# Optimization experiments

Hardware: AMD Instinct MI355X
Metric: run time of the kernel (lower is better)

## Reference

```python
import jax, jax.numpy as jnp
import numpy as np

B, L, D_MODEL, H = 2, 2048, 1024, 16
D_HEAD = D_MODEL // H
NEG = -1e9


def setup_inputs() -> dict:
    key = jax.random.key(0)
    ks = jax.random.split(key, 8)
    q = jax.random.normal(ks[0], (B, L, D_MODEL), dtype=jnp.float32)
    k = jax.random.normal(ks[1], (B, L, D_MODEL), dtype=jnp.float32)
    v = jax.random.normal(ks[2], (B, L, D_MODEL), dtype=jnp.float32)
    # causal mask: True where attention is disallowed (masked_fill semantics)
    mask = jnp.broadcast_to(jnp.triu(jnp.ones((L, L), dtype=bool), k=1), (B, L, L))
    s = 1.0 / np.sqrt(D_MODEL)
    Wq = jax.random.normal(ks[3], (D_MODEL, D_MODEL), dtype=jnp.float32) * s
    Wk = jax.random.normal(ks[4], (D_MODEL, D_MODEL), dtype=jnp.float32) * s
    Wv = jax.random.normal(ks[5], (D_MODEL, D_MODEL), dtype=jnp.float32) * s
    Wo = jax.random.normal(ks[6], (D_MODEL, D_MODEL), dtype=jnp.float32) * s
    return {"q": q, "k": k, "v": v, "mask": mask,
            "Wq": Wq, "Wk": Wk, "Wv": Wv, "Wo": Wo}


def reference(q, k, v, mask, Wq, Wk, Wv, Wo):
    # projections (Linear, bias=False)
    qh = (q @ Wq).reshape(B, L, H, D_HEAD)
    kh = (k @ Wk).reshape(B, L, H, D_HEAD)
    vh = (v @ Wv).reshape(B, L, H, D_HEAD)
    # per-head scores: contiguous d_model slices == head reshape
    scores = jnp.einsum("bqhd,bkhd->bhqk", qh, kh)
    scores = jnp.where(mask[:, None, :, :], NEG, scores)
    # NOTE: original applies softmax FIRST, then divides by sqrt(d_head)
    weights = jax.nn.softmax(scores, axis=-1) / np.sqrt(D_HEAD).astype(np.float32)
    att = jnp.einsum("bhqk,bkhd->bqhd", weights, vh).reshape(B, L, D_MODEL)
    # dropout is identity in eval mode
    return att @ Wo
```

## Files before the change

### kernel.cpp

```cpp
#include <hip/hip_runtime.h>
#include <hip/hip_bf16.h>

#define BATCH  2
#define SEQ    2048
#define DMODEL 1024
#define NHEAD  16
#define DHEAD  64

typedef _Float16 f16x4 __attribute__((ext_vector_type(4)));
typedef _Float16 f16x8 __attribute__((ext_vector_type(8)));
typedef float    f32x4 __attribute__((ext_vector_type(4)));

union H16 { unsigned short u; _Float16 f; };
__device__ __forceinline__ _Float16 u2h(unsigned short u) { H16 c; c.u = u; return c.f; }
__device__ __forceinline__ unsigned short h2u(_Float16 f) { H16 c; c.f = f; return c.u; }

__device__ __forceinline__ void gll16(const void* g, void* l) {
    __builtin_amdgcn_global_load_lds(
        (const __attribute__((address_space(1))) void*)g,
        (__attribute__((address_space(3))) void*)l, 16, 0, 0);
}

__device__ __forceinline__ float dpp_max16(float x) {
    float t;
    t = __int_as_float(__builtin_amdgcn_update_dpp(0, __float_as_int(x), 0xB1, 0xF, 0xF, true));
    x = fmaxf(x, t);
    t = __int_as_float(__builtin_amdgcn_update_dpp(0, __float_as_int(x), 0x4E, 0xF, 0xF, true));
    x = fmaxf(x, t);
    t = __int_as_float(__builtin_amdgcn_update_dpp(0, __float_as_int(x), 0x124, 0xF, 0xF, true));
    x = fmaxf(x, t);
    t = __int_as_float(__builtin_amdgcn_update_dpp(0, __float_as_int(x), 0x128, 0xF, 0xF, true));
    x = fmaxf(x, t);
    return x;
}

__device__ __forceinline__ void pack_body(const float* __restrict__ W,
                                          _Float16* __restrict__ Phi,
                                          _Float16* __restrict__ Plo)
{
    const int n0 = blockIdx.x * 64;
    const int k0 = blockIdx.y * 64;
    const int t  = threadIdx.x;
    const int nl = t & 63;
    const int kc = (t >> 6) * 16;
    const int n  = n0 + nl;
    const int sw = (n & 3) ^ ((n >> 2) & 3);

    _Float16 hi[16], lo[16];
#pragma unroll
    for (int i = 0; i < 16; i++) {
        float x = W[(size_t)(k0 + kc + i) * DMODEL + n] * 32.0f;
        _Float16 h = (_Float16)x;
        hi[i] = h;
        lo[i] = (_Float16)(x - (float)h);
    }
#pragma unroll
    for (int cc = 0; cc < 2; cc++) {
        const int kk = kc + cc * 8;
        const int g  = kk >> 5;
        const int c  = (kk >> 3) & 3;
        const size_t off = (size_t)n * DMODEL + k0 + g * 32 + ((c ^ sw) << 3);
        *(f16x8*)&Phi[off] = *(f16x8*)&hi[cc * 8];
        if (Plo) *(f16x8*)&Plo[off] = *(f16x8*)&lo[cc * 8];
    }
}

__global__ __launch_bounds__(256) void pack_qkv(const float* __restrict__ Wq,
                                                const float* __restrict__ Wk,
                                                const float* __restrict__ Wv,
                                                _Float16* qhiT, _Float16* qloT,
                                                _Float16* khiT, _Float16* kloT,
                                                _Float16* vhiT)
{
    const int z = blockIdx.z;
    pack_body(z == 0 ? Wq : z == 1 ? Wk : Wv,
              z == 0 ? qhiT : z == 1 ? khiT : vhiT,
              z == 0 ? qloT : z == 1 ? kloT : nullptr);
}

__global__ __launch_bounds__(256) void pack_one(const float* __restrict__ W,
                                                _Float16* Phi)
{
    pack_body(W, Phi, nullptr);
}

template <int SPLIT, typename CT>
__global__ __launch_bounds__(256) void gemm_mfma(const float* __restrict__ A0,
                                                 const float* __restrict__ A1,
                                                 const _Float16* __restrict__ Bh0,
                                                 const _Float16* __restrict__ Bl0,
                                                 const _Float16* __restrict__ Bh1,
                                                 const _Float16* __restrict__ Bl1,
                                                 CT* __restrict__ C0,
                                                 CT* __restrict__ C1,
                                                 _Float16* __restrict__ Kh,
                                                 _Float16* __restrict__ Kl,
                                                 int N, int K)
{
    constexpr int ASZ = 128 * 40;
    constexpr int BSZ = 128 * 32;
    constexpr int AHI = 0;
    constexpr int ALO = ASZ;
    constexpr int BHI = ASZ * (SPLIT == 3 ? 2 : 1);
    constexpr int BLO = BHI + 2 * BSZ;
    constexpr int TOT = BHI + 2 * BSZ * (SPLIT == 3 ? 2 : 1);
    __shared__ __align__(16) _Float16 smem[TOT];

    const float*    A  = blockIdx.z ? A1 : A0;
    const _Float16* Bh = blockIdx.z ? Bh1 : Bh0;
    const _Float16* Bl = blockIdx.z ? Bl1 : Bl0;
    CT*             C  = blockIdx.z ? C1 : C0;

    const int m0 = blockIdx.x * 128;
    const int n0 = blockIdx.y * 128;
    const int t    = threadIdx.x;
    const int wave = t >> 6;
    const int lane = t & 63;
    const int quad = lane >> 4;
    const int col  = lane & 15;
    const int wm   = (wave & 1) * 64;
    const int wn   = (wave >> 1) * 64;

    const int ar  = t >> 1;
    const int akc = (t & 1) * 16;
    const float* Ap = A + (size_t)(m0 + ar) * K + akc;

    const _Float16* BhSrc = Bh + (size_t)(n0 + wave * 32 + (lane >> 2)) * K + (lane & 3) * 8;
    const _Float16* BlSrc = (SPLIT == 3)
        ? Bl + (size_t)(n0 + wave * 32 + (lane >> 2)) * K + (lane & 3) * 8 : nullptr;

    const int qe8 = (quad ^ ((col & 3) ^ ((col >> 2) & 3))) * 8;

    f32x4 acc[4][4];
#pragma unroll
    for (int mt = 0; mt < 4; mt++)
#pragma unroll
        for (int nt = 0; nt < 4; nt++) acc[mt][nt] = (f32x4){0.f, 0.f, 0.f, 0.f};

    float av[16];
    auto loadA = [&](int k0) {
#pragma unroll
        for (int g = 0; g < 4; g++) {
            float4 x = *(const float4*)(Ap + k0 + g * 4);
            av[g * 4 + 0] = x.x; av[g * 4 + 1] = x.y;
            av[g * 4 + 2] = x.z; av[g * 4 + 3] = x.w;
        }
    };
    auto issueB = [&](int k0, int buf) {
        _Float16* d0 = &smem[BHI + buf * BSZ + wave * 1024];
        gll16(BhSrc + k0, d0);
        gll16(BhSrc + (size_t)16 * K + k0, d0 + 512);
        if constexpr (SPLIT == 3) {
            _Float16* d1 = &smem[BLO + buf * BSZ + wave * 1024];
            gll16(BlSrc + k0, d1);
            gll16(BlSrc + (size_t)16 * K + k0, d1 + 512);
        }
    };
    auto storeA = [&]() {
#pragma unroll
        for (int g = 0; g < 2; g++) {
            f16x8 h, l;
#pragma unroll
            for (int j = 0; j < 8; j++) {
                float x = av[g * 8 + j];
                _Float16 hh = (_Float16)x;
                h[j] = hh;
                l[j] = (_Float16)(x - (float)hh);
            }
            *(f16x8*)&smem[AHI + ar * 40 + akc + g * 8] = h;
            if constexpr (SPLIT == 3)
                *(f16x8*)&smem[ALO + ar * 40 + akc + g * 8] = l;
        }
    };

    loadA(0);
    issueB(0, 0);

    int buf = 0;
    for (int k0 = 0; k0 < K; k0 += 32, buf ^= 1) {
        storeA();
        __syncthreads();

        if (k0 + 32 < K) { issueB(k0 + 32, buf ^ 1); loadA(k0 + 32); }

        f16x8 ah[4], al[4], bh[4], bl[4];
#pragma unroll
        for (int mt = 0; mt < 4; mt++) {
            ah[mt] = *(f16x8*)&smem[AHI + (wm + mt * 16 + col) * 40 + quad * 8];
            if constexpr (SPLIT == 3)
                al[mt] = *(f16x8*)&smem[ALO + (wm + mt * 16 + col) * 40 + quad * 8];
        }
#pragma unroll
        for (int nt = 0; nt < 4; nt++) {
            bh[nt] = *(f16x8*)&smem[BHI + buf * BSZ + (wn + nt * 16 + col) * 32 + qe8];
            if constexpr (SPLIT == 3)
                bl[nt] = *(f16x8*)&smem[BLO + buf * BSZ + (wn + nt * 16 + col) * 32 + qe8];
        }
#pragma unroll
        for (int nt = 0; nt < 4; nt++)
#pragma unroll
            for (int mt = 0; mt < 4; mt++) {
                acc[mt][nt] = __builtin_amdgcn_mfma_f32_16x16x32_f16(ah[mt], bh[nt], acc[mt][nt], 0, 0, 0);
                if constexpr (SPLIT == 3) {
                    acc[mt][nt] = __builtin_amdgcn_mfma_f32_16x16x32_f16(ah[mt], bl[nt], acc[mt][nt], 0, 0, 0);
                    acc[mt][nt] = __builtin_amdgcn_mfma_f32_16x16x32_f16(al[mt], bh[nt], acc[mt][nt], 0, 0, 0);
                }
            }
        __syncthreads();
    }

    const float inv = 1.0f / 32.0f;
#pragma unroll
    for (int mt = 0; mt < 4; mt++)
#pragma unroll
        for (int nt = 0; nt < 4; nt++)
#pragma unroll
            for (int r = 0; r < 4; r++) {
                float val = acc[mt][nt][r] * inv;
                size_t idx = (size_t)(m0 + wm + mt * 16 + quad * 4 + r) * N
                           + n0 + wn + nt * 16 + col;
                if constexpr (SPLIT == 3) {
                    _Float16 h = (_Float16)val;
                    if (blockIdx.z == 0) {
                        _Float16 l = (_Float16)(val - (float)h);
                        C[idx] = (unsigned)h2u(h) | ((unsigned)h2u(l) << 16);
                    } else {
                        Kh[idx] = h;
                        Kl[idx] = (_Float16)(val - (float)h);
                    }
                } else if constexpr (__is_same(CT, _Float16)) {
                    C[idx] = (_Float16)val;
                } else {
                    C[idx] = val;
                }
            }
}

#define AKH 0
#define AKL 8192
#define AVT 16384
#define AVT_SIZE (64 * 72 + 64)
#define AP  (AVT + AVT_SIZE)
#define AP_WAVE (16 * 72)
#define ATOT (AP + 4 * AP_WAVE)

__global__ __launch_bounds__(256) void attn_mfma(unsigned* __restrict__ qa,
                                                 const _Float16* __restrict__ khi,
                                                 const _Float16* __restrict__ klo,
                                                 const _Float16* __restrict__ vh)
{
    __shared__ __align__(16) _Float16 smem[ATOT];

    const int i  = blockIdx.x;
    const int j  = i >> 3;
    const int bh = (i & 7) + ((j & 3) << 3);
    const int qt = (SEQ / 64 - 1) - (j >> 2);
    const int b  = bh >> 4;
    const int h  = bh & 15;
    const int qb = qt * 64;

    const int t    = threadIdx.x;
    const int wave = t >> 6;
    const int lane = t & 63;
    const int quad = lane >> 4;
    const int col  = lane & 15;

    const size_t bbase = (size_t)b * SEQ * DMODEL + (size_t)h * DHEAD;
    const _Float16* vb_ptr = vh + bbase;

    const int qm = qb + wave * 16 + col;
    f16x8 qhi[2], qlo[2];
    {
        const unsigned* qp = qa + bbase + (size_t)qm * DMODEL + quad * 8;
#pragma unroll
        for (int kt = 0; kt < 2; kt++) {
            uint4 u0 = *(const uint4*)(qp + kt * 32);
            uint4 u1 = *(const uint4*)(qp + kt * 32 + 4);
            unsigned us[8] = {u0.x, u0.y, u0.z, u0.w, u1.x, u1.y, u1.z, u1.w};
#pragma unroll
            for (int jj = 0; jj < 8; jj++) {
                qhi[kt][jj] = u2h((unsigned short)(us[jj] & 0xffffu));
                qlo[kt][jj] = u2h((unsigned short)(us[jj] >> 16));
            }
        }
    }

    const int rl0  = wave * 16 + (lane >> 3);
    const int kswz = (lane & 7) ^ ((lane >> 3) & 7);
    const size_t kbase = ((size_t)b * SEQ + rl0) * DMODEL + h * DHEAD + (kswz << 3);

    auto issueK = [&](int kb, int buf) {
        const _Float16* sh = khi + kbase + (size_t)kb * DMODEL;
        const _Float16* sl = klo + kbase + (size_t)kb * DMODEL;
        _Float16* dh = &smem[AKH + buf * 4096 + wave * 1024];
        _Float16* dl = &smem[AKL + buf * 4096 + wave * 1024];
        gll16(sh, dh);
        gll16(sh + (size_t)8 * DMODEL, dh + 512);
        gll16(sl, dl);
        gll16(sl + (size_t)8 * DMODEL, dl + 512);
    };

    const int srow = t >> 2;
    const int sdg  = (t & 3) << 4;
    const int vswz = (t & 3) * 16;
    f16x8 pv[2];
    auto loadV = [&](int kb) {
        const _Float16* vp = vb_ptr + (size_t)(kb + srow) * DMODEL + sdg;
        pv[0] = *(const f16x8*)vp;
        pv[1] = *(const f16x8*)(vp + 8);
    };

    f16x8 kOnes;
#pragma unroll
    for (int jj = 0; jj < 8; jj++) kOnes[jj] = (_Float16)1.0f;

    float m_i[4];
    f32x4 l4 = (f32x4){0.f, 0.f, 0.f, 0.f};
    f32x4 o[4];
#pragma unroll
    for (int r = 0; r < 4; r++) m_i[r] = -1e30f;
#pragma unroll
    for (int dt = 0; dt < 4; dt++) o[dt] = (f32x4){0.f, 0.f, 0.f, 0.f};

    const int wq0 = qb + wave * 16;
    _Float16* Pw = &smem[AP + wave * AP_WAVE];
    const int cs = col & 7;

    loadV(0);
    issueK(0, 0);

    int buf = 0;
    for (int kb = 0; kb <= qb; kb += 64, buf ^= 1) {
        __syncthreads();

#pragma unroll
        for (int jj = 0; jj < 8; jj++) {
            smem[AVT + (sdg + jj    ) * 72 + vswz + srow] = pv[0][jj];
            smem[AVT + (sdg + 8 + jj) * 72 + vswz + srow] = pv[1][jj];
        }
        __syncthreads();

        if (kb + 64 <= qb) { issueK(kb + 64, buf ^ 1); loadV(kb + 64); }

        f32x4 acc[4];
#pragma unroll
        for (int ct = 0; ct < 4; ct++) acc[ct] = (f32x4){0.f, 0.f, 0.f, 0.f};
#pragma unroll
        for (int kt = 0; kt < 2; kt++) {
#pragma unroll
            for (int ct = 0; ct < 4; ct++) {
                const int off = (ct * 16 + col) * 64 + ((((kt << 2) | quad) ^ cs) << 3);
                f16x8 bhi = *(f16x8*)&smem[AKH + buf * 4096 + off];
                f16x8 blo = *(f16x8*)&smem[AKL + buf * 4096 + off];
                acc[ct] = __builtin_amdgcn_mfma_f32_16x16x32_f16(qhi[kt], bhi, acc[ct], 0, 0, 0);
                acc[ct] = __builtin_amdgcn_mfma_f32_16x16x32_f16(qhi[kt], blo, acc[ct], 0, 0, 0);
                acc[ct] = __builtin_amdgcn_mfma_f32_16x16x32_f16(qlo[kt], bhi, acc[ct], 0, 0, 0);
            }
        }

        const bool need_mask = (kb + 63 > wq0);
#pragma unroll
        for (int r = 0; r < 4; r++) {
            const int qrow = wq0 + quad * 4 + r;
            float s0 = acc[0][r], s1 = acc[1][r], s2 = acc[2][r], s3 = acc[3][r];
            if (need_mask) {
                s0 = (kb +  0 + col <= qrow) ? s0 : -1e30f;
                s1 = (kb + 16 + col <= qrow) ? s1 : -1e30f;
                s2 = (kb + 32 + col <= qrow) ? s2 : -1e30f;
                s3 = (kb + 48 + col <= qrow) ? s3 : -1e30f;
            }
            float rm = dpp_max16(fmaxf(fmaxf(s0, s1), fmaxf(s2, s3)));
            const float mnew  = fmaxf(m_i[r], rm);
            const float alpha = __expf(m_i[r] - mnew);
            const float p0 = __expf(s0 - mnew), p1 = __expf(s1 - mnew);
            const float p2 = __expf(s2 - mnew), p3 = __expf(s3 - mnew);
            m_i[r] = mnew;
            l4[r] *= alpha;
#pragma unroll
            for (int dt = 0; dt < 4; dt++) o[dt][r] *= alpha;
            const int prow = quad * 4 + r;
            Pw[prow * 72 + col     ] = (_Float16)p0;
            Pw[prow * 72 + col + 16] = (_Float16)p1;
            Pw[prow * 72 + col + 32] = (_Float16)p2;
            Pw[prow * 72 + col + 48] = (_Float16)p3;
        }

#pragma unroll
        for (int kt = 0; kt < 2; kt++) {
            f16x8 a = *(f16x8*)&Pw[col * 72 + kt * 32 + quad * 8];
            l4 = __builtin_amdgcn_mfma_f32_16x16x32_f16(a, kOnes, l4, 0, 0, 0);
#pragma unroll
            for (int dt = 0; dt < 4; dt++) {
                f16x8 bv = *(f16x8*)&smem[AVT + (dt * 16 + col) * 72 + (dt & 3) * 16 + kt * 32 + quad * 8];
                o[dt] = __builtin_amdgcn_mfma_f32_16x16x32_f16(a, bv, o[dt], 0, 0, 0);
            }
        }
    }

#pragma unroll
    for (int r = 0; r < 4; r++) {
        const float inv = 1.0f / (l4[r] * 8.0f);
        const int q = wq0 + quad * 4 + r;
        unsigned* op = qa + bbase + (size_t)q * DMODEL;
#pragma unroll
        for (int dt = 0; dt < 4; dt++)
            op[dt * 16 + col] = __float_as_uint(o[dt][r] * inv);
    }
}

extern "C" void kernel_launch(void* const* d_in, const int* in_sizes, int n_in,
                              void* d_out, int out_size, void* d_ws, size_t ws_size,
                              hipStream_t stream)
{
    const float* q  = (const float*)d_in[0];
    const float* k  = (const float*)d_in[1];
    const float* v  = (const float*)d_in[2];
    const float* Wq = (const float*)d_in[4];
    const float* Wk = (const float*)d_in[5];
    const float* Wv = (const float*)d_in[6];
    const float* Wo = (const float*)d_in[7];
    float* out = (float*)d_out;

    const int    M   = BATCH * SEQ;
    const size_t npe = (size_t)M * DMODEL;
    const size_t PW  = (size_t)DMODEL * DMODEL;

    unsigned* qh    = (unsigned*)d_ws;
    _Float16* khi_p = (_Float16*)(qh + npe);
    _Float16* klo_p = khi_p + npe;

    _Float16* dh    = (_Float16*)d_out;
    _Float16* qhiT  = dh;
    _Float16* qloT  = dh + PW;
    _Float16* khiT  = dh + 2 * PW;
    _Float16* kloT  = dh + 3 * PW;
    _Float16* vhiT  = dh + 4 * PW;
    _Float16* vh    = dh;
    _Float16* wohiT = khi_p;

    dim3 b256(256);
    dim3 pk(DMODEL / 64, DMODEL / 64, 3);
    dim3 pk1(DMODEL / 64, DMODEL / 64, 1);
    dim3 gqk(M / 128, DMODEL / 128, 2);
    dim3 g1(M / 128, DMODEL / 128, 1);
    dim3 agrid(1024);

    pack_qkv<<<pk, b256, 0, stream>>>(Wq, Wk, Wv, qhiT, qloT, khiT, kloT, vhiT);
    gemm_mfma<3, unsigned><<<gqk, b256, 0, stream>>>(q, k, qhiT, qloT, khiT, kloT,
                                                     qh, nullptr, khi_p, klo_p,
                                                     DMODEL, DMODEL);
    gemm_mfma<1, _Float16><<<g1, b256, 0, stream>>>(v, v, vhiT, nullptr, vhiT, nullptr,
                                                    vh, vh, nullptr, nullptr,
                                                    DMODEL, DMODEL);
    attn_mfma<<<agrid, b256, 0, stream>>>(qh, khi_p, klo_p, vh);
    pack_one<<<pk1, b256, 0, stream>>>(Wo, wohiT);
    gemm_mfma<1, float><<<g1, b256, 0, stream>>>((const float*)qh, (const float*)qh,
                                                 wohiT, nullptr, wohiT, nullptr,
                                                 out, out, nullptr, nullptr,
                                                 DMODEL, DMODEL);
}
```

Before: 333.0 us.

## Double-buffer the A tile in LDS with an XOR swizzle, one barrier per step

The A operand tile of the projection GEMM now gets two LDS buffers like B. The next tile's converted values are stored after the MFMAs of the current step, so each k-step needs only one __syncthreads instead of two. The A layout changes from a padded 40-element row stride to a 32-element stride with the same XOR swizzle B uses, to avoid bank conflicts. This uses more LDS per block (the A region doubles), which could lower occupancy.

Result: faster. 303.2 us (-9.0%).

```diff
diff --git a/kernel.cpp b/kernel.cpp
--- a/kernel.cpp
+++ b/kernel.cpp
@@ -97,13 +97,12 @@
                                                  _Float16* __restrict__ Kl,
                                                  int N, int K)
 {
-    constexpr int ASZ = 128 * 40;
-    constexpr int BSZ = 128 * 32;
+    constexpr int PB  = 128 * 32;
     constexpr int AHI = 0;
-    constexpr int ALO = ASZ;
-    constexpr int BHI = ASZ * (SPLIT == 3 ? 2 : 1);
-    constexpr int BLO = BHI + 2 * BSZ;
-    constexpr int TOT = BHI + 2 * BSZ * (SPLIT == 3 ? 2 : 1);
+    constexpr int ALO = 2 * PB;
+    constexpr int BHI = (SPLIT == 3 ? 4 : 2) * PB;
+    constexpr int BLO = BHI + 2 * PB;
+    constexpr int TOT = (SPLIT == 3 ? 8 : 4) * PB;
     __shared__ __align__(16) _Float16 smem[TOT];
 
     const float*    A  = blockIdx.z ? A1 : A0;
@@ -123,6 +122,7 @@
 
     const int ar  = t >> 1;
     const int akc = (t & 1) * 16;
+    const int asw = (ar & 3) ^ ((ar >> 2) & 3);
     const float* Ap = A + (size_t)(m0 + ar) * K + akc;
 
     const _Float16* BhSrc = Bh + (size_t)(n0 + wave * 32 + (lane >> 2)) * K + (lane & 3) * 8;
@@ -147,16 +147,16 @@
         }
     };
     auto issueB = [&](int k0, int buf) {
-        _Float16* d0 = &smem[BHI + buf * BSZ + wave * 1024];
+        _Float16* d0 = &smem[BHI + buf * PB + wave * 1024];
         gll16(BhSrc + k0, d0);
         gll16(BhSrc + (size_t)16 * K + k0, d0 + 512);
         if constexpr (SPLIT == 3) {
-            _Float16* d1 = &smem[BLO + buf * BSZ + wave * 1024];
+            _Float16* d1 = &smem[BLO + buf * PB + wave * 1024];
             gll16(BlSrc + k0, d1);
             gll16(BlSrc + (size_t)16 * K + k0, d1 + 512);
         }
     };
-    auto storeA = [&]() {
+    auto storeA = [&](int sbuf) {
 #pragma unroll
         for (int g = 0; g < 2; g++) {
             f16x8 h, l;
@@ -167,34 +167,40 @@
                 h[j] = hh;
                 l[j] = (_Float16)(x - (float)hh);
             }
-            *(f16x8*)&smem[AHI + ar * 40 + akc + g * 8] = h;
+            const int off = ar * 32 + ((((akc >> 3) + g) ^ asw) << 3);
+            *(f16x8*)&smem[AHI + sbuf * PB + off] = h;
             if constexpr (SPLIT == 3)
-                *(f16x8*)&smem[ALO + ar * 40 + akc + g * 8] = l;
+                *(f16x8*)&smem[ALO + sbuf * PB + off] = l;
         }
     };
 
     loadA(0);
     issueB(0, 0);
+    storeA(0);
+    __syncthreads();
 
     int buf = 0;
     for (int k0 = 0; k0 < K; k0 += 32, buf ^= 1) {
-        storeA();
-        __syncthreads();
-
-        if (k0 + 32 < K) { issueB(k0 + 32, buf ^ 1); loadA(k0 + 32); }
+        const bool pre = (k0 + 32 < K);
+        if (pre) {
+            loadA(k0 + 32);
+            issueB(k0 + 32, buf ^ 1);
+        }
 
         f16x8 ah[4], al[4], bh[4], bl[4];
 #pragma unroll
         for (int mt = 0; mt < 4; mt++) {
-            ah[mt] = *(f16x8*)&smem[AHI + (wm + mt * 16 + col) * 40 + quad * 8];
+            const int arow = (wm + mt * 16 + col) * 32 + qe8;
+            ah[mt] = *(f16x8*)&smem[AHI + buf * PB + arow];
             if constexpr (SPLIT == 3)
-                al[mt] = *(f16x8*)&smem[ALO + (wm + mt * 16 + col) * 40 + quad * 8];
+                al[mt] = *(f16x8*)&smem[ALO + buf * PB + arow];
         }
 #pragma unroll
         for (int nt = 0; nt < 4; nt++) {
-            bh[nt] = *(f16x8*)&smem[BHI + buf * BSZ + (wn + nt * 16 + col) * 32 + qe8];
+            const int brow = (wn + nt * 16 + col) * 32 + qe8;
+            bh[nt] = *(f16x8*)&smem[BHI + buf * PB + brow];
             if constexpr (SPLIT == 3)
-                bl[nt] = *(f16x8*)&smem[BLO + buf * BSZ + (wn + nt * 16 + col) * 32 + qe8];
+                bl[nt] = *(f16x8*)&smem[BLO + buf * PB + brow];
         }
 #pragma unroll
         for (int nt = 0; nt < 4; nt++)
@@ -206,6 +212,8 @@
                     acc[mt][nt] = __builtin_amdgcn_mfma_f32_16x16x32_f16(al[mt], bh[nt], acc[mt][nt], 0, 0, 0);
                 }
             }
+
+        if (pre) storeA(buf ^ 1);
         __syncthreads();
     }
 
```
